# Optimization experiments

Measured on AMD Instinct MI355X. Metric: run time of the kernel, lower is better.

## Reference

```python
import jax, jax.numpy as jnp
import numpy as np

KS = 3            # kernel_size
DILS = (1, 2, 4)  # dilation_list == padding_list
EPS = 1e-5        # BN eps


def _unfold3(x, d):
    # emulate F.unfold(kernel=3, dilation=d, padding=d, stride=1).view(b, c, 9, h, w)
    b, c, h, w = x.shape
    xp = jnp.pad(x, ((0, 0), (0, 0), (d, d), (d, d)))
    pats = [xp[:, :, i * d:i * d + h, j * d:j * d + w] for i in range(KS) for j in range(KS)]
    return jnp.stack(pats, axis=2)


def _conv1x1(x, w, b):
    return jnp.einsum('bchw,oc->bohw', x, w) + b[None, :, None, None]


def _bn_relu(x, g, be, m, v):
    s = g / jnp.sqrt(v + EPS)
    return jax.nn.relu(x * s[None, :, None, None] + (be - m * s)[None, :, None, None])


def _proj(x, w1, b1, g1, be1, m1, v1, w2, b2, g2, be2, m2, v2):
    h = _bn_relu(_conv1x1(x, w1, b1), g1, be1, m1, v1)
    return _bn_relu(_conv1x1(h, w2, b2), g2, be2, m2, v2)


def setup_inputs():
    key = jax.random.key(0)
    Cin, Ck, Cv, Cout = 512, 256, 256, 512
    B, H, W = 4, 64, 64
    ks = iter(jax.random.split(key, 48))

    def nrm(shape, s=0.02):
        return jax.random.normal(next(ks), shape, jnp.float32) * s

    def bn(c):
        return (jnp.ones((c,), jnp.float32) + nrm((c,), 0.1),  # gamma
                nrm((c,), 0.1),                                 # beta
                nrm((c,), 0.1),                                 # running mean
                jax.random.uniform(next(ks), (c,), jnp.float32, 0.5, 1.5))  # running var

    inp = {"x": jax.random.normal(next(ks), (B, Cin, H, W), jnp.float32)}
    for p in ("k", "q"):
        g1, be1, m1, v1 = bn(Ck)
        g2, be2, m2, v2 = bn(Ck)
        inp.update({
            p + "1_w": nrm((Ck, Cin)), p + "1_b": nrm((Ck,)),
            p + "1_g": g1, p + "1_be": be1, p + "1_m": m1, p + "1_v": v1,
            p + "2_w": nrm((Ck, Ck)), p + "2_b": nrm((Ck,)),
            p + "2_g": g2, p + "2_be": be2, p + "2_m": m2, p + "2_v": v2,
        })
    inp["v_w"] = nrm((Cv, Cin)); inp["v_b"] = nrm((Cv,))
    inp["w_w"] = nrm((Cout, Cv)); inp["w_b"] = nrm((Cout,))
    return inp


def reference(x,
              k1_w, k1_b, k1_g, k1_be, k1_m, k1_v,
              k2_w, k2_b, k2_g, k2_be, k2_m, k2_v,
              q1_w, q1_b, q1_g, q1_be, q1_m, q1_v,
              q2_w, q2_b, q2_g, q2_be, q2_m, q2_v,
              v_w, v_b, w_w, w_b):
    # scale == 1: MaxPool2d(1x1-equivalent) and final bilinear resize are identities.
    value = _conv1x1(x, v_w, v_b)                                  # (b,cv,h,w)
    keyf = _proj(x, k1_w, k1_b, k1_g, k1_be, k1_m, k1_v,
                 k2_w, k2_b, k2_g, k2_be, k2_m, k2_v)              # (b,ck,h,w)
    query = _proj(x, q1_w, q1_b, q1_g, q1_be, q1_m, q1_v,
                  q2_w, q2_b, q2_g, q2_be, q2_m, q2_v)             # (b,ck,h,w)
    uk = jnp.concatenate([_unfold3(keyf, d) for d in DILS], axis=2)   # (b,ck,27,h,w)
    uv = jnp.concatenate([_unfold3(value, d) for d in DILS], axis=2)  # (b,cv,27,h,w)
    sim = jnp.sum(uk * query[:, :, None], axis=1, keepdims=True)      # (b,1,27,h,w)
    sim = jax.nn.softmax(sim, axis=2)
    context = jnp.sum(sim * uv, axis=2)                               # (b,cv,h,w)
    return _conv1x1(context, w_w, w_b)
```

## Files before the change

### kernel.cpp

```cpp
#include <hip/hip_runtime.h>

#define HW   4096
#define Hh   64
#define Ww   64
#define NB   27
#define EPSBN 1e-5f

typedef _Float16 f16x8 __attribute__((ext_vector_type(8)));
typedef _Float16 f16x4 __attribute__((ext_vector_type(4)));
typedef _Float16 f16x2 __attribute__((ext_vector_type(2)));
typedef float    f32x4 __attribute__((ext_vector_type(4)));

__device__ __forceinline__ void gld_lds16(const void* g, void* l) {
    __builtin_amdgcn_global_load_lds(
        (const __attribute__((address_space(1))) unsigned int*)g,
        (__attribute__((address_space(3))) unsigned int*)l, 16, 0, 0);
}

__global__ __launch_bounds__(256)
void prep_kernel(const float* s0, const float* s1, const float* s2,
                 const float* s3, const float* s4, const float* s5,
                 _Float16* d0, _Float16* d1, _Float16* d2,
                 _Float16* d3, _Float16* d4, _Float16* d5)
{
    const int bid = blockIdx.x;
    const int j  = bid >> 6;
    const int bx = bid & 63;
    const float* s = j==0?s0: j==1?s1: j==2?s2: j==3?s3: j==4?s4: s5;
    _Float16*  d = j==0?d0: j==1?d1: j==2?d2: j==3?d3: j==4?d4: d5;
    const int  n = (j==3 || j==4) ? 65536 : 131072;
    const int  i = (bx * 256 + threadIdx.x) * 8;
    if (i < n) {
        f16x8 h;
        #pragma unroll
        for (int k = 0; k < 8; ++k) h[k] = (_Float16)s[i + k];
        *(f16x8*)(d + i) = h;
    }
}

struct GJob {
    const _Float16* in;
    const float*    xf;
    const _Float16* w;
    const float* b; const float* g; const float* be; const float* m; const float* v;
    _Float16* oh;
    float*    of;
};

__global__ __launch_bounds__(256)
void gemm128(GJob J0, GJob J1, GJob J2, int nmb0, int nmb01, int nmbTot,
             int K, int JO, int mode)
{
    __shared__ _Float16 As[2][128 * 64];
    __shared__ _Float16 Bs[2][128 * 64];

    const int tid  = threadIdx.x;
    const int lane = tid & 63;
    const int w    = tid >> 6;
    const int lr   = lane & 15;
    const int lg   = lane >> 4;
    const int wm   = w & 1;
    const int wn   = w >> 1;

    const int bid = blockIdx.x;
    const int xcd = bid & 7;
    const int jj  = bid >> 3;
    const int nb  = xcd * 16 + jj / nmbTot;
    const int mb  = jj % nmbTot;

    const bool i0 = mb < nmb0;
    const bool i1 = !i0 && mb < nmb01;
#define SELJ(f) (i0 ? J0.f : (i1 ? J1.f : J2.f))
    const _Float16* Jin = SELJ(in);
    const float*    Jxf = SELJ(xf);
    const _Float16* Jw  = SELJ(w);
    const float* Jb  = SELJ(b);
    const float* Jg  = SELJ(g);
    const float* Jbe = SELJ(be);
    const float* Jm  = SELJ(m);
    const float* Jv  = SELJ(v);
    _Float16* Joh = SELJ(oh);
    float*    Jof = SELJ(of);
#undef SELJ
    const int obase = (mb - (i0 ? 0 : (i1 ? nmb0 : nmb01))) * 128;

    const int rowS = w * 32 + (lane >> 3);
    const int scol = (((lane & 7) ^ (lane >> 3)) << 3);
    const _Float16* aSrc = Jw + (size_t)(obase + rowS) * K + scol;
    const _Float16* bSrc = Jin ? (Jin + (size_t)(nb * 128 + rowS) * K + scol) : nullptr;

    const int h    = w & 1;
    const int q    = w >> 1;
    const int brow = h * 64 + lane;
    const int bxor = (brow & 7) << 4;
    const float* xbase = nullptr;
    if (Jxf) {
        const int bb = nb >> 5;
        const int pp = (nb & 31) * 128 + h * 64 + lane;
        xbase = Jxf + (size_t)bb * 512 * HW + pp;
    }

    float fr[4][8];

    auto STAGE_A = [&](int buf, int rd) {
        const int kb = rd * 64;
        char* aD = (char*)&As[buf][0] + w * 4096;
        #pragma unroll
        for (int j2 = 0; j2 < 4; ++j2)
            gld_lds16(aSrc + (size_t)j2 * 8 * K + kb, aD + j2 * 1024);
    };
    auto STAGE_B_LDS = [&](int buf, int rd) {
        const int kb = rd * 64;
        char* bD = (char*)&Bs[buf][0] + w * 4096;
        #pragma unroll
        for (int j2 = 0; j2 < 4; ++j2)
            gld_lds16(bSrc + (size_t)j2 * 8 * K + kb, bD + j2 * 1024);
    };
    auto ISSUE_BX = [&](int rd) {
        const int kb = rd * 64 + q * 32;
        #pragma unroll
        for (int g2 = 0; g2 < 4; ++g2)
            #pragma unroll
            for (int i2 = 0; i2 < 8; ++i2)
                fr[g2][i2] = xbase[(size_t)(kb + g2 * 8 + i2) * HW];
    };
    auto WRITE_BX = [&](int buf) {
        #pragma unroll
        for (int g2 = 0; g2 < 4; ++g2) {
            f16x8 hv;
            #pragma unroll
            for (int i2 = 0; i2 < 8; ++i2) hv[i2] = (_Float16)fr[g2][i2];
            *(f16x8*)((char*)&Bs[buf][0] + brow * 128 + ((q * 64 + g2 * 16) ^ bxor)) = hv;
        }
    };

    f32x4 acc[4][4] = {};
    const int nr = K >> 6;

    if (Jxf) { ISSUE_BX(0); WRITE_BX(0); }
    else     { STAGE_B_LDS(0, 0); }
    STAGE_A(0, 0);
    __syncthreads();

    int cur = 0;
    for (int rd = 0; rd < nr; ++rd) {
        const bool more = (rd + 1 < nr);
        if (more) {
            STAGE_A(cur ^ 1, rd + 1);
            if (Jxf) ISSUE_BX(rd + 1);
            else     STAGE_B_LDS(cur ^ 1, rd + 1);
        }
        #pragma unroll
        for (int ks = 0; ks < 2; ++ks) {
            const int colx = (ks * 64 + lg * 16) ^ ((lr & 7) << 4);
            f16x8 afr[4], bfr[4];
            #pragma unroll
            for (int t = 0; t < 4; ++t) {
                afr[t] = *(const f16x8*)((const char*)&As[cur][0] + (wm * 64 + t * 16 + lr) * 128 + colx);
                bfr[t] = *(const f16x8*)((const char*)&Bs[cur][0] + (wn * 64 + t * 16 + lr) * 128 + colx);
            }
            #pragma unroll
            for (int ai = 0; ai < 4; ++ai)
                #pragma unroll
                for (int bj = 0; bj < 4; ++bj)
                    acc[ai][bj] = __builtin_amdgcn_mfma_f32_16x16x32_f16(
                        afr[ai], bfr[bj], acc[ai][bj], 0, 0, 0);
        }
        if (Jxf && more) WRITE_BX(cur ^ 1);
        __syncthreads();
        cur ^= 1;
    }

    const int relu = (Jg != nullptr);
    #pragma unroll
    for (int ai = 0; ai < 4; ++ai) {
        const int o4 = obase + wm * 64 + ai * 16 + lg * 4;
        float sc[4], of_[4];
        #pragma unroll
        for (int r = 0; r < 4; ++r) {
            const int o = o4 + r;
            if (Jg) { float s = Jg[o] * rsqrtf(Jv[o] + EPSBN); sc[r] = s; of_[r] = fmaf(Jb[o] - Jm[o], s, Jbe[o]); }
            else    { sc[r] = 1.f; of_[r] = Jb[o]; }
        }
        #pragma unroll
        for (int bj = 0; bj < 4; ++bj) {
            const int pg = nb * 128 + wn * 64 + bj * 16 + lr;
            float vv[4];
            #pragma unroll
            for (int r = 0; r < 4; ++r) {
                float t = fmaf(acc[ai][bj][r], sc[r], of_[r]);
                vv[r] = relu ? fmaxf(t, 0.f) : t;
            }
            if (mode == 0) {
                f16x4 hh;
                #pragma unroll
                for (int r = 0; r < 4; ++r) hh[r] = (_Float16)vv[r];
                *(f16x4*)(Joh + (size_t)pg * JO + o4) = hh;
            } else {
                #pragma unroll
                for (int r = 0; r < 4; ++r)
                    Jof[((size_t)(pg >> 12) * JO + o4 + r) * HW + (pg & 4095)] = vv[r];
            }
        }
    }
}

__global__ __launch_bounds__(256)
void attn_fused(const _Float16* __restrict__ keyT, const _Float16* __restrict__ qryT,
                const _Float16* __restrict__ valT, _Float16* __restrict__ ctxT)
{
    const int tid  = threadIdx.x;
    const int slot = tid & 31;
    const int b    = blockIdx.y;
    const int p    = blockIdx.x * 8 + (tid >> 5);
    const int y    = p >> 6;
    const int xc   = p & 63;

    int   idx[NB];
    float valf[NB];
    #pragma unroll
    for (int n = 0; n < NB; ++n) {
        const int d  = (n < 9) ? 1 : (n < 18 ? 2 : 4);
        const int i  = (n / 3) % 3 - 1;
        const int j  = n % 3 - 1;
        const int yy = y + i * d, xx = xc + j * d;
        const bool ok = ((unsigned)yy < (unsigned)Hh) && ((unsigned)xx < (unsigned)Ww);
        idx[n]  = min(max(yy, 0), Hh - 1) * Ww + min(max(xx, 0), Ww - 1);
        valf[n] = ok ? 1.f : 0.f;
    }

    const size_t base = (size_t)b * HW * 256 + slot * 8;
    const f16x8 q8 = *(const f16x8*)(qryT + base + (size_t)p * 256);

    f16x2 qp[4];
    qp[0] = __builtin_shufflevector(q8, q8, 0, 1);
    qp[1] = __builtin_shufflevector(q8, q8, 2, 3);
    qp[2] = __builtin_shufflevector(q8, q8, 4, 5);
    qp[3] = __builtin_shufflevector(q8, q8, 6, 7);

    float sim[NB];
    #pragma unroll
    for (int n = 0; n < NB; ++n) {
        const f16x8 k8 = *(const f16x8*)(keyT + base + (size_t)idx[n] * 256);
        float s = 0.f;
        s = __builtin_amdgcn_fdot2(__builtin_shufflevector(k8, k8, 0, 1), qp[0], s, false);
        s = __builtin_amdgcn_fdot2(__builtin_shufflevector(k8, k8, 2, 3), qp[1], s, false);
        s = __builtin_amdgcn_fdot2(__builtin_shufflevector(k8, k8, 4, 5), qp[2], s, false);
        s = __builtin_amdgcn_fdot2(__builtin_shufflevector(k8, k8, 6, 7), qp[3], s, false);
        sim[n] = s;
    }

    #pragma unroll
    for (int n = 0; n < NB; ++n) {
        float s = sim[n];
        s += __shfl_xor(s, 1);
        s += __shfl_xor(s, 2);
        s += __shfl_xor(s, 4);
        s += __shfl_xor(s, 8);
        s += __shfl_xor(s, 16);
        sim[n] = s * valf[n];
    }

    float mx = sim[0];
    #pragma unroll
    for (int n = 1; n < NB; ++n) mx = fmaxf(mx, sim[n]);
    float sum = 0.f;
    #pragma unroll
    for (int n = 0; n < NB; ++n) { sim[n] = __expf(sim[n] - mx); sum += sim[n]; }
    const float inv = 1.f / sum;
    #pragma unroll
    for (int n = 0; n < NB; ++n) sim[n] = sim[n] * inv * valf[n];

    float acc[8];
    #pragma unroll
    for (int i = 0; i < 8; ++i) acc[i] = 0.f;
    #pragma unroll
    for (int n = 0; n < NB; ++n) {
        const f16x8 v8 = *(const f16x8*)(valT + base + (size_t)idx[n] * 256);
        const float w = sim[n];
        #pragma unroll
        for (int i = 0; i < 8; ++i) acc[i] = fmaf(w, (float)v8[i], acc[i]);
    }

    f16x8 h;
    #pragma unroll
    for (int i = 0; i < 8; ++i) h[i] = (_Float16)acc[i];
    *(f16x8*)(ctxT + base + (size_t)p * 256) = h;
}

extern "C" void kernel_launch(void* const* d_in, const int* in_sizes, int n_in,
                              void* d_out, int out_size, void* d_ws, size_t ws_size,
                              hipStream_t stream)
{
    (void)in_sizes; (void)n_in; (void)out_size; (void)ws_size;
    const float* x     = (const float*)d_in[0];
    const float* k1_w  = (const float*)d_in[1];
    const float* k1_b  = (const float*)d_in[2];
    const float* k1_g  = (const float*)d_in[3];
    const float* k1_be = (const float*)d_in[4];
    const float* k1_m  = (const float*)d_in[5];
    const float* k1_v  = (const float*)d_in[6];
    const float* k2_w  = (const float*)d_in[7];
    const float* k2_b  = (const float*)d_in[8];
    const float* k2_g  = (const float*)d_in[9];
    const float* k2_be = (const float*)d_in[10];
    const float* k2_m  = (const float*)d_in[11];
    const float* k2_v  = (const float*)d_in[12];
    const float* q1_w  = (const float*)d_in[13];
    const float* q1_b  = (const float*)d_in[14];
    const float* q1_g  = (const float*)d_in[15];
    const float* q1_be = (const float*)d_in[16];
    const float* q1_m  = (const float*)d_in[17];
    const float* q1_v  = (const float*)d_in[18];
    const float* q2_w  = (const float*)d_in[19];
    const float* q2_b  = (const float*)d_in[20];
    const float* q2_g  = (const float*)d_in[21];
    const float* q2_be = (const float*)d_in[22];
    const float* q2_m  = (const float*)d_in[23];
    const float* q2_v  = (const float*)d_in[24];
    const float* v_w   = (const float*)d_in[25];
    const float* v_b   = (const float*)d_in[26];
    const float* w_w   = (const float*)d_in[27];
    const float* w_b   = (const float*)d_in[28];

    _Float16* hw = (_Float16*)d_ws;
    const size_t SH = (size_t)4 * HW * 256;
    _Float16* wv_h  = hw;
    _Float16* wk1_h = wv_h  + 131072;
    _Float16* wq1_h = wk1_h + 131072;
    _Float16* wk2_h = wq1_h + 131072;
    _Float16* wq2_h = wk2_h + 65536;
    _Float16* ww_h  = wq2_h + 65536;
    _Float16* k1T   = ww_h  + 131072;
    _Float16* q1T   = k1T + SH;
    _Float16* valT  = q1T + SH;
    _Float16* ctxT  = valT + SH;
    _Float16* keyPC = ctxT + SH;
    _Float16* qryPC = keyPC + SH;

    prep_kernel<<<384, 256, 0, stream>>>(v_w, k1_w, q1_w, k2_w, q2_w, w_w,
                                         wv_h, wk1_h, wq1_h, wk2_h, wq2_h, ww_h);

    GJob jv  = { nullptr, x, wv_h,  v_b,  nullptr, nullptr, nullptr, nullptr, valT,  nullptr };
    GJob jk1 = { nullptr, x, wk1_h, k1_b, k1_g, k1_be, k1_m, k1_v,            k1T,   nullptr };
    GJob jq1 = { nullptr, x, wq1_h, q1_b, q1_g, q1_be, q1_m, q1_v,            q1T,   nullptr };
    GJob jk2 = { k1T, nullptr, wk2_h, k2_b, k2_g, k2_be, k2_m, k2_v,          keyPC, nullptr };
    GJob jq2 = { q1T, nullptr, wq2_h, q2_b, q2_g, q2_be, q2_m, q2_v,          qryPC, nullptr };
    GJob jw  = { ctxT, nullptr, ww_h, w_b,  nullptr, nullptr, nullptr, nullptr, nullptr, (float*)d_out };

    gemm128<<<768, 256, 0, stream>>>(jv, jk1, jq1, 2, 4, 6, 512, 256, 0);
    gemm128<<<512, 256, 0, stream>>>(jk2, jq2, jq2, 2, 4, 4, 256, 256, 0);
    attn_fused<<<dim3(512, 4), 256, 0, stream>>>(keyPC, qryPC, valT, ctxT);
    gemm128<<<512, 256, 0, stream>>>(jw, jw, jw, 4, 4, 4, 256, 512, 2);
}
```

Baseline: 96.13 us.

## Shrink GEMM M-tile to 64 and drop LDS double buffering

The GEMM kernel now uses a 64x128 output tile instead of 128x128, halving A-tile LDS and per-wave accumulators and doubling the grid size for all three GEMM launches. The double-buffered prefetch pipeline is replaced by a single buffer with two barriers per K step, with loads and compute serialized. The aim is more blocks and occupancy (smaller LDS and register footprint) to hide latency. The cost is lower arithmetic intensity, more redundant loads of the x/B operand, and no overlap of loads with MFMA.

```diff
diff --git a/kernel.cpp b/kernel.cpp
--- a/kernel.cpp
+++ b/kernel.cpp
@@ -48,11 +48,11 @@
 };
 
 __global__ __launch_bounds__(256)
-void gemm128(GJob J0, GJob J1, GJob J2, int nmb0, int nmb01, int nmbTot,
-             int K, int JO, int mode)
+void gemm64(GJob J0, GJob J1, GJob J2, int nmb0, int nmb01, int nmbTot,
+            int K, int JO, int mode)
 {
-    __shared__ _Float16 As[2][128 * 64];
-    __shared__ _Float16 Bs[2][128 * 64];
+    __shared__ _Float16 As[64 * 64];
+    __shared__ _Float16 Bs[128 * 64];
 
     const int tid  = threadIdx.x;
     const int lane = tid & 63;
@@ -82,99 +82,75 @@
     _Float16* Joh = SELJ(oh);
     float*    Jof = SELJ(of);
 #undef SELJ
-    const int obase = (mb - (i0 ? 0 : (i1 ? nmb0 : nmb01))) * 128;
-
-    const int rowS = w * 32 + (lane >> 3);
+    const int obase = (mb - (i0 ? 0 : (i1 ? nmb0 : nmb01))) * 64;
+
     const int scol = (((lane & 7) ^ (lane >> 3)) << 3);
-    const _Float16* aSrc = Jw + (size_t)(obase + rowS) * K + scol;
-    const _Float16* bSrc = Jin ? (Jin + (size_t)(nb * 128 + rowS) * K + scol) : nullptr;
-
-    const int h    = w & 1;
-    const int q    = w >> 1;
-    const int brow = h * 64 + lane;
-    const int bxor = (brow & 7) << 4;
+    const int rowA = w * 16 + (lane >> 3);
+    const _Float16* aSrc = Jw + (size_t)(obase + rowA) * K + scol;
+    const int rowB = w * 32 + (lane >> 3);
+    const _Float16* bSrc = Jin ? (Jin + (size_t)(nb * 128 + rowB) * K + scol) : nullptr;
+
+    const int xrow = tid & 127;
+    const int chq  = tid >> 7;
     const float* xbase = nullptr;
     if (Jxf) {
         const int bb = nb >> 5;
-        const int pp = (nb & 31) * 128 + h * 64 + lane;
+        const int pp = (nb & 31) * 128 + xrow;
         xbase = Jxf + (size_t)bb * 512 * HW + pp;
     }
-
-    float fr[4][8];
-
-    auto STAGE_A = [&](int buf, int rd) {
+    const int bxorw = (xrow & 7) << 4;
+
+    f32x4 acc[2][4] = {};
+    const int nr = K >> 6;
+
+    for (int rd = 0; rd < nr; ++rd) {
         const int kb = rd * 64;
-        char* aD = (char*)&As[buf][0] + w * 4096;
-        #pragma unroll
-        for (int j2 = 0; j2 < 4; ++j2)
-            gld_lds16(aSrc + (size_t)j2 * 8 * K + kb, aD + j2 * 1024);
-    };
-    auto STAGE_B_LDS = [&](int buf, int rd) {
-        const int kb = rd * 64;
-        char* bD = (char*)&Bs[buf][0] + w * 4096;
-        #pragma unroll
-        for (int j2 = 0; j2 < 4; ++j2)
-            gld_lds16(bSrc + (size_t)j2 * 8 * K + kb, bD + j2 * 1024);
-    };
-    auto ISSUE_BX = [&](int rd) {
-        const int kb = rd * 64 + q * 32;
-        #pragma unroll
-        for (int g2 = 0; g2 < 4; ++g2)
-            #pragma unroll
-            for (int i2 = 0; i2 < 8; ++i2)
-                fr[g2][i2] = xbase[(size_t)(kb + g2 * 8 + i2) * HW];
-    };
-    auto WRITE_BX = [&](int buf) {
-        #pragma unroll
-        for (int g2 = 0; g2 < 4; ++g2) {
-            f16x8 hv;
-            #pragma unroll
-            for (int i2 = 0; i2 < 8; ++i2) hv[i2] = (_Float16)fr[g2][i2];
-            *(f16x8*)((char*)&Bs[buf][0] + brow * 128 + ((q * 64 + g2 * 16) ^ bxor)) = hv;
+        __syncthreads();
+        gld_lds16(aSrc + kb,                  (char*)As + w * 2048);
+        gld_lds16(aSrc + (size_t)8 * K + kb,  (char*)As + w * 2048 + 1024);
+        if (Jxf) {
+            float fr[32];
+            #pragma unroll
+            for (int g2 = 0; g2 < 4; ++g2)
+                #pragma unroll
+                for (int i2 = 0; i2 < 8; ++i2)
+                    fr[g2 * 8 + i2] = xbase[(size_t)(kb + chq * 32 + g2 * 8 + i2) * HW];
+            #pragma unroll
+            for (int g2 = 0; g2 < 4; ++g2) {
+                f16x8 hv;
+                #pragma unroll
+                for (int i2 = 0; i2 < 8; ++i2) hv[i2] = (_Float16)fr[g2 * 8 + i2];
+                *(f16x8*)((char*)Bs + xrow * 128 + ((chq * 64 + g2 * 16) ^ bxorw)) = hv;
+            }
+        } else {
+            #pragma unroll
+            for (int j2 = 0; j2 < 4; ++j2)
+                gld_lds16(bSrc + (size_t)j2 * 8 * K + kb, (char*)Bs + w * 4096 + j2 * 1024);
         }
-    };
-
-    f32x4 acc[4][4] = {};
-    const int nr = K >> 6;
-
-    if (Jxf) { ISSUE_BX(0); WRITE_BX(0); }
-    else     { STAGE_B_LDS(0, 0); }
-    STAGE_A(0, 0);
-    __syncthreads();
-
-    int cur = 0;
-    for (int rd = 0; rd < nr; ++rd) {
-        const bool more = (rd + 1 < nr);
-        if (more) {
-            STAGE_A(cur ^ 1, rd + 1);
-            if (Jxf) ISSUE_BX(rd + 1);
-            else     STAGE_B_LDS(cur ^ 1, rd + 1);
-        }
+        __syncthreads();
+
         #pragma unroll
         for (int ks = 0; ks < 2; ++ks) {
             const int colx = (ks * 64 + lg * 16) ^ ((lr & 7) << 4);
-            f16x8 afr[4], bfr[4];
-            #pragma unroll
-            for (int t = 0; t < 4; ++t) {
-                afr[t] = *(const f16x8*)((const char*)&As[cur][0] + (wm * 64 + t * 16 + lr) * 128 + colx);
-                bfr[t] = *(const f16x8*)((const char*)&Bs[cur][0] + (wn * 64 + t * 16 + lr) * 128 + colx);
-            }
-            #pragma unroll
-            for (int ai = 0; ai < 4; ++ai)
+            f16x8 afr[2], bfr[4];
+            afr[0] = *(const f16x8*)((const char*)As + (wm * 32 + lr) * 128 + colx);
+            afr[1] = *(const f16x8*)((const char*)As + (wm * 32 + 16 + lr) * 128 + colx);
+            #pragma unroll
+            for (int t = 0; t < 4; ++t)
+                bfr[t] = *(const f16x8*)((const char*)Bs + (wn * 64 + t * 16 + lr) * 128 + colx);
+            #pragma unroll
+            for (int ai = 0; ai < 2; ++ai)
                 #pragma unroll
                 for (int bj = 0; bj < 4; ++bj)
                     acc[ai][bj] = __builtin_amdgcn_mfma_f32_16x16x32_f16(
                         afr[ai], bfr[bj], acc[ai][bj], 0, 0, 0);
         }
-        if (Jxf && more) WRITE_BX(cur ^ 1);
-        __syncthreads();
-        cur ^= 1;
     }
 
     const int relu = (Jg != nullptr);
     #pragma unroll
-    for (int ai = 0; ai < 4; ++ai) {
-        const int o4 = obase + wm * 64 + ai * 16 + lg * 4;
+    for (int ai = 0; ai < 2; ++ai) {
+        const int o4 = obase + wm * 32 + ai * 16 + lg * 4;
         float sc[4], of_[4];
         #pragma unroll
         for (int r = 0; r < 4; ++r) {
@@ -348,8 +324,8 @@
     GJob jq2 = { q1T, nullptr, wq2_h, q2_b, q2_g, q2_be, q2_m, q2_v,          qryPC, nullptr };
     GJob jw  = { ctxT, nullptr, ww_h, w_b,  nullptr, nullptr, nullptr, nullptr, nullptr, (float*)d_out };
 
-    gemm128<<<768, 256, 0, stream>>>(jv, jk1, jq1, 2, 4, 6, 512, 256, 0);
-    gemm128<<<512, 256, 0, stream>>>(jk2, jq2, jq2, 2, 4, 4, 256, 256, 0);
+    gemm64<<<1536, 256, 0, stream>>>(jv, jk1, jq1, 4, 8, 12, 512, 256, 0);
+    gemm64<<<1024, 256, 0, stream>>>(jk2, jq2, jq2, 4, 8, 8, 256, 256, 0);
     attn_fused<<<dim3(512, 4), 256, 0, stream>>>(keyPC, qryPC, valT, ctxT);
-    gemm128<<<512, 256, 0, stream>>>(jw, jw, jw, 4, 4, 4, 256, 512, 2);
-}
+    gemm64<<<1024, 256, 0, stream>>>(jw, jw, jw, 8, 8, 8, 256, 512, 2);
+}
```

Result: slower. 103.9 us (+8.1%).
